# Kernel tuning notes

Hardware: AMD Instinct MI355X
Metric: run time of the kernel (lower is better)

Reference implementation:

```python
import jax, jax.numpy as jnp
import numpy as np

N_NODES = 100000
N_EDGES = 3200000
IN_CH = 128
HID = 16


def setup_inputs() -> dict:
    key = jax.random.key(0)
    ks = jax.random.split(key, 6)
    x = jax.random.normal(ks[0], (N_NODES, IN_CH), dtype=jnp.float32)
    edge_index = jax.random.randint(ks[1], (2, N_EDGES), 0, N_NODES, dtype=jnp.int32)
    W1 = jax.random.normal(ks[2], (IN_CH, HID), dtype=jnp.float32) / np.sqrt(IN_CH)
    b1 = jnp.zeros((HID,), jnp.float32)
    W2 = jax.random.normal(ks[3], (HID, HID), dtype=jnp.float32) / np.sqrt(HID)
    b2 = jnp.zeros((HID,), jnp.float32)
    Wl = jax.random.normal(ks[4], (HID, 1), dtype=jnp.float32) / np.sqrt(HID)
    bl = jnp.zeros((1,), jnp.float32)
    return {"x": x, "edge_index": edge_index, "W1": W1, "b1": b1,
            "W2": W2, "b2": b2, "Wl": Wl, "bl": bl}


def _gcn_conv(x, row, col, dinv, W, b, n_nodes):
    # PyG GCNConv: out[col] += d^{-1/2}[row] * d^{-1/2}[col] * (x @ W)[row]; + bias
    h = x @ W                                   # [N, C_out] small matmul
    norm = dinv[row] * dinv[col]                # [E+N] edge weights (with self-loops)
    msg = h[row] * norm[:, None]                # gather + scale
    out = jax.ops.segment_sum(msg, col, num_segments=n_nodes)  # scatter-add
    return out + b


def reference(x, edge_index, W1, b1, W2, b2, Wl, bl):
    n = x.shape[0]
    loops = jnp.arange(n, dtype=edge_index.dtype)
    row = jnp.concatenate([edge_index[0], loops])  # sources (with self-loops)
    col = jnp.concatenate([edge_index[1], loops])  # targets
    # symmetric normalization degrees computed on A + I at target index
    deg = jax.ops.segment_sum(jnp.ones(col.shape[0], x.dtype), col, num_segments=n)
    dinv = jnp.where(deg > 0, jax.lax.rsqrt(deg), 0.0)
    h = jax.nn.relu(_gcn_conv(x, row, col, dinv, W1, b1, n))
    h = jax.nn.relu(_gcn_conv(h, row, col, dinv, W2, b2, n))
    return h @ Wl + bl
```

## Files before the change

### kernel.cpp

```cpp
#include <hip/hip_runtime.h>

#define IN_CH 128
#define HID 16
#define SHIFT 8
#define CA 16384
#define SCAN_B 512
#define MAXNB 512

typedef int vint4 __attribute__((ext_vector_type(4)));


__global__ __launch_bounds__(256) void histA_kernel(
    const int* __restrict__ col, int* __restrict__ histT, int e, int NB, int nba) {
    __shared__ int hist[MAXNB];
    int j = blockIdx.x, t = threadIdx.x;
    for (int b = t; b < NB; b += 256) hist[b] = 0;
    __syncthreads();
    int e4 = e >> 2;
    const int4* c4p = (const int4*)col;
#pragma unroll
    for (int k = 0; k < CA / 1024; ++k) {
        int i4 = j * (CA / 4) + k * 256 + t;
        if (i4 < e4) {
            int4 c = c4p[i4];
            atomicAdd(&hist[c.x >> SHIFT], 1);
            atomicAdd(&hist[c.y >> SHIFT], 1);
            atomicAdd(&hist[c.z >> SHIFT], 1);
            atomicAdd(&hist[c.w >> SHIFT], 1);
        }
    }
    if (j == gridDim.x - 1) {
        for (int i = (e & ~3) + t; i < e; i += 256) atomicAdd(&hist[col[i] >> SHIFT], 1);
    }
    __syncthreads();
    for (int b = t; b < NB; b += 256) histT[b * nba + j] = hist[b];
}


__global__ __launch_bounds__(SCAN_B) void scan1_kernel(
    const int* __restrict__ in, int* __restrict__ out, int* __restrict__ bsum, int m) {
    __shared__ int s[SCAN_B];
    int t = threadIdx.x;
    int i = blockIdx.x * SCAN_B + t;
    int v = (i < m) ? in[i] : 0;
    s[t] = v;
    __syncthreads();
    for (int off = 1; off < SCAN_B; off <<= 1) {
        int a = (t >= off) ? s[t - off] : 0;
        __syncthreads();
        s[t] += a;
        __syncthreads();
    }
    if (i < m) out[i] = s[t] - v;
    if (t == SCAN_B - 1) bsum[blockIdx.x] = s[t];
}

__global__ __launch_bounds__(SCAN_B) void scan2_kernel(int* __restrict__ bsum, int nb) {
    __shared__ int s[SCAN_B];
    int t = threadIdx.x;
    int v = (t < nb) ? bsum[t] : 0;
    s[t] = v;
    __syncthreads();
    for (int off = 1; off < SCAN_B; off <<= 1) {
        int a = (t >= off) ? s[t - off] : 0;
        __syncthreads();
        s[t] += a;
        __syncthreads();
    }
    if (t < nb) bsum[t] = s[t] - v;
}


__global__ __launch_bounds__(256) void scatterA_kernel(
    const int* __restrict__ row, const int* __restrict__ col,
    const int* __restrict__ histTs, const int* __restrict__ bsum2,
    int* __restrict__ tmp, int e, int NB, int nba) {
    __shared__ int cur[MAXNB];
    int j = blockIdx.x, t = threadIdx.x;
    for (int b = t; b < NB; b += 256) {
        int idx = b * nba + j;
        cur[b] = histTs[idx] + bsum2[idx >> 9];
    }
    __syncthreads();
    int e4 = e >> 2;
    const int4* c4p = (const int4*)col;
    const int4* r4p = (const int4*)row;
#pragma unroll
    for (int k = 0; k < CA / 1024; ++k) {
        int i4 = j * (CA / 4) + k * 256 + t;
        if (i4 < e4) {
            int4 c = c4p[i4];
            int4 r = r4p[i4];
            int pos;
            pos = atomicAdd(&cur[c.x >> SHIFT], 1); tmp[pos] = (r.x << 8) | (c.x & 255);
            pos = atomicAdd(&cur[c.y >> SHIFT], 1); tmp[pos] = (r.y << 8) | (c.y & 255);
            pos = atomicAdd(&cur[c.z >> SHIFT], 1); tmp[pos] = (r.z << 8) | (c.z & 255);
            pos = atomicAdd(&cur[c.w >> SHIFT], 1); tmp[pos] = (r.w << 8) | (c.w & 255);
        }
    }
    if (j == gridDim.x - 1) {
        for (int i = (e & ~3) + t; i < e; i += 256) {
            int c = col[i], r = row[i];
            int pos = atomicAdd(&cur[c >> SHIFT], 1);
            tmp[pos] = (r << 8) | (c & 255);
        }
    }
}


__global__ __launch_bounds__(256) void bucketC_kernel(
    const int* __restrict__ tmp, const int* __restrict__ histTs, const int* __restrict__ bsum2,
    int* __restrict__ row_ptr, int* __restrict__ pcnt, int* __restrict__ bktTot,
    float* __restrict__ dinv, int n, int e, int NB, int nba) {
    __shared__ int hcnt[256];
    __shared__ int scn[256];
    int b = blockIdx.x, t = threadIdx.x;
    int i0 = b * nba, i1 = (b + 1) * nba;
    int bs = histTs[i0] + bsum2[i0 >> 9];
    int be = (b + 1 < NB) ? (histTs[i1] + bsum2[i1 >> 9]) : e;
    hcnt[t] = 0;
    __syncthreads();
    for (int i = bs + t; i < be; i += 256) atomicAdd(&hcnt[tmp[i] & 255], 1);
    __syncthreads();
    int cnt = hcnt[t];
    int pc = (cnt + 7) & ~7;
    scn[t] = pc;
    __syncthreads();
    for (int off = 1; off < 256; off <<= 1) {
        int a = (t >= off) ? scn[t - off] : 0;
        __syncthreads();
        scn[t] += a;
        __syncthreads();
    }
    int excl = scn[t] - pc;
    int node = (b << SHIFT) + t;
    if (node < n) {
        row_ptr[node] = excl;
        pcnt[node] = pc;
        dinv[node] = rsqrtf((float)(cnt + 1));
    }
    if (t == 255) bktTot[b] = scn[255];
    if (b == 0 && t == 0) dinv[n] = 0.0f;
}

__global__ __launch_bounds__(SCAN_B) void scanB_kernel(
    int* __restrict__ bktTot, int* __restrict__ row_ptr, int NB, int n) {
    __shared__ int s[SCAN_B];
    int t = threadIdx.x;
    int v = (t < NB) ? bktTot[t] : 0;
    s[t] = v;
    __syncthreads();
    for (int off = 1; off < SCAN_B; off <<= 1) {
        int a = (t >= off) ? s[t - off] : 0;
        __syncthreads();
        s[t] += a;
        __syncthreads();
    }
    if (t < NB) bktTot[t] = s[t] - v;
    if (t == SCAN_B - 1) row_ptr[n] = s[t];
}


__global__ __launch_bounds__(256) void bucketD_kernel(
    const int* __restrict__ tmp, const int* __restrict__ histTs, const int* __restrict__ bsum2,
    const int* __restrict__ bktTot, const int* __restrict__ pcnt,
    int* __restrict__ row_ptr, int* __restrict__ pk,
    int n, int e, int NB, int nba) {
    __shared__ int cur[256];
    int b = blockIdx.x, t = threadIdx.x;
    int i0 = b * nba, i1 = (b + 1) * nba;
    int bs = histTs[i0] + bsum2[i0 >> 9];
    int be = (b + 1 < NB) ? (histTs[i1] + bsum2[i1 >> 9]) : e;
    int node = (b << SHIFT) + t;
    int rp = 0, pc = 0;
    if (node < n) {
        rp = bktTot[b] + row_ptr[node];
        pc = pcnt[node];
        row_ptr[node] = rp;
    }
    cur[t] = rp;
    __syncthreads();
    for (int i = bs + t; i < be; i += 256) {
        int u = tmp[i];
        int pos = atomicAdd(&cur[u & 255], 1);
        pk[pos] = u >> 8;
    }
    __syncthreads();
    int pe = rp + pc;
    for (int p = cur[t]; p < pe; ++p) pk[p] = n;
}


__global__ __launch_bounds__(256) void gemm1_kernel(
    const float* __restrict__ x, const float* __restrict__ W1,
    const float* __restrict__ dinv, float* __restrict__ hs, int n) {
    __shared__ float4 swl[512];
    int t = threadIdx.x;
#pragma unroll
    for (int i = t; i < 512; i += 256) {
        float4 v = ((const float4*)W1)[i];
        int k = i >> 2, q = i & 3;
        int kp = ((k & 31) << 2) | (k >> 5);
        swl[kp * 4 + q] = v;
    }
    __syncthreads();
    int gid = blockIdx.x * 256 + t;
    int r = gid >> 2;
    int sub = gid & 3;
    if (r > n) return;
    float4 xv[8];
    if (r < n) {
        const float4* xp = (const float4*)(x + (size_t)r * IN_CH + sub * 32);
#pragma unroll
        for (int j = 0; j < 8; ++j) xv[j] = xp[j];
    } else {
#pragma unroll
        for (int j = 0; j < 8; ++j) xv[j] = make_float4(0.f, 0.f, 0.f, 0.f);
    }
    float acc[16];
#pragma unroll
    for (int c = 0; c < 16; ++c) acc[c] = 0.f;
#pragma unroll
    for (int j = 0; j < 8; ++j) {
#pragma unroll
        for (int q = 0; q < 4; ++q) {
            int jq = j * 4 + q;
            float xs = (q == 0) ? xv[j].x : (q == 1) ? xv[j].y : (q == 2) ? xv[j].z : xv[j].w;
            const float4* wp = &swl[(jq * 4 + sub) * 4];
            float4 w0 = wp[0], w1 = wp[1], w2 = wp[2], w3 = wp[3];
            acc[0]  = fmaf(xs, w0.x, acc[0]);
            acc[1]  = fmaf(xs, w0.y, acc[1]);
            acc[2]  = fmaf(xs, w0.z, acc[2]);
            acc[3]  = fmaf(xs, w0.w, acc[3]);
            acc[4]  = fmaf(xs, w1.x, acc[4]);
            acc[5]  = fmaf(xs, w1.y, acc[5]);
            acc[6]  = fmaf(xs, w1.z, acc[6]);
            acc[7]  = fmaf(xs, w1.w, acc[7]);
            acc[8]  = fmaf(xs, w2.x, acc[8]);
            acc[9]  = fmaf(xs, w2.y, acc[9]);
            acc[10] = fmaf(xs, w2.z, acc[10]);
            acc[11] = fmaf(xs, w2.w, acc[11]);
            acc[12] = fmaf(xs, w3.x, acc[12]);
            acc[13] = fmaf(xs, w3.y, acc[13]);
            acc[14] = fmaf(xs, w3.z, acc[14]);
            acc[15] = fmaf(xs, w3.w, acc[15]);
        }
    }
#pragma unroll
    for (int c = 0; c < 16; ++c) {
        acc[c] += __shfl_xor(acc[c], 1);
        acc[c] += __shfl_xor(acc[c], 2);
    }
    float dg = dinv[r];
    float4 o;
    o.x = dg * acc[sub * 4 + 0];
    o.y = dg * acc[sub * 4 + 1];
    o.z = dg * acc[sub * 4 + 2];
    o.w = dg * acc[sub * 4 + 3];
    ((float4*)hs)[(size_t)r * 4 + sub] = o;
}


__global__ __launch_bounds__(256) void agg1_kernel(
    const float* __restrict__ hs, const int* __restrict__ row_ptr,
    const int* __restrict__ pk, const float* __restrict__ dinv,
    const float* __restrict__ b1, const float* __restrict__ W2,
    float* __restrict__ hs2, int n) {
    int t = threadIdx.x;
    int node = blockIdx.x * 64 + (t >> 2);
    int sub = t & 3;
    if (node >= n) return;
    const float4* h4 = (const float4*)hs;
    float4 self = h4[(size_t)node * 4 + sub];
    float cx = self.x, cy = self.y, cz = self.z, cw = self.w;
    int beg = __builtin_nontemporal_load(row_ptr + node);
    int end = __builtin_nontemporal_load(row_ptr + node + 1);
    for (int j = beg; j < end; j += 8) {
        vint4 p0 = __builtin_nontemporal_load((const vint4*)(pk + j));
        vint4 p1 = __builtin_nontemporal_load((const vint4*)(pk + j + 4));
        float4 v0 = h4[(size_t)p0.x * 4 + sub];
        float4 v1 = h4[(size_t)p0.y * 4 + sub];
        float4 v2 = h4[(size_t)p0.z * 4 + sub];
        float4 v3 = h4[(size_t)p0.w * 4 + sub];
        float4 v4 = h4[(size_t)p1.x * 4 + sub];
        float4 v5 = h4[(size_t)p1.y * 4 + sub];
        float4 v6 = h4[(size_t)p1.z * 4 + sub];
        float4 v7 = h4[(size_t)p1.w * 4 + sub];
        cx += ((v0.x + v1.x) + (v2.x + v3.x)) + ((v4.x + v5.x) + (v6.x + v7.x));
        cy += ((v0.y + v1.y) + (v2.y + v3.y)) + ((v4.y + v5.y) + (v6.y + v7.y));
        cz += ((v0.z + v1.z) + (v2.z + v3.z)) + ((v4.z + v5.z) + (v6.z + v7.z));
        cw += ((v0.w + v1.w) + (v2.w + v3.w)) + ((v4.w + v5.w) + (v6.w + v7.w));
    }
    float dg = dinv[node];
    float4 b1v = *(const float4*)(b1 + (sub << 2));
    float ax = fmaxf(fmaf(dg, cx, b1v.x), 0.f);
    float ay = fmaxf(fmaf(dg, cy, b1v.y), 0.f);
    float az = fmaxf(fmaf(dg, cz, b1v.z), 0.f);
    float aw = fmaxf(fmaf(dg, cw, b1v.w), 0.f);
    float ox = 0.f, oy = 0.f, oz = 0.f, ow = 0.f;
#pragma unroll
    for (int r = 0; r < 4; ++r) {
        float fx = __shfl_xor(ax, r);
        float fy = __shfl_xor(ay, r);
        float fz = __shfl_xor(az, r);
        float fw = __shfl_xor(aw, r);
        int kb = (sub ^ r) << 2;
        const float* wp = W2 + kb * HID + (sub << 2);
        float4 w0 = *(const float4*)(wp);
        float4 w1 = *(const float4*)(wp + HID);
        float4 w2 = *(const float4*)(wp + 2 * HID);
        float4 w3 = *(const float4*)(wp + 3 * HID);
        ox += fx * w0.x + fy * w1.x + fz * w2.x + fw * w3.x;
        oy += fx * w0.y + fy * w1.y + fz * w2.y + fw * w3.y;
        oz += fx * w0.z + fy * w1.z + fz * w2.z + fw * w3.z;
        ow += fx * w0.w + fy * w1.w + fz * w2.w + fw * w3.w;
    }
    float4 o; o.x = dg * ox; o.y = dg * oy; o.z = dg * oz; o.w = dg * ow;
    ((float4*)hs2)[(size_t)node * 4 + sub] = o;
}

__global__ __launch_bounds__(256) void agg2_kernel(
    const float* __restrict__ hs2, const int* __restrict__ row_ptr,
    const int* __restrict__ pk, const float* __restrict__ dinv,
    const float* __restrict__ b2, const float* __restrict__ Wl,
    const float* __restrict__ bl, float* __restrict__ out, int n) {
    int t = threadIdx.x;
    int node = blockIdx.x * 64 + (t >> 2);
    int sub = t & 3;
    if (node >= n) return;
    const float4* h4 = (const float4*)hs2;
    float4 self = h4[(size_t)node * 4 + sub];
    float cx = self.x, cy = self.y, cz = self.z, cw = self.w;
    int beg = __builtin_nontemporal_load(row_ptr + node);
    int end = __builtin_nontemporal_load(row_ptr + node + 1);
    for (int j = beg; j < end; j += 8) {
        vint4 p0 = __builtin_nontemporal_load((const vint4*)(pk + j));
        vint4 p1 = __builtin_nontemporal_load((const vint4*)(pk + j + 4));
        float4 v0 = h4[(size_t)p0.x * 4 + sub];
        float4 v1 = h4[(size_t)p0.y * 4 + sub];
        float4 v2 = h4[(size_t)p0.z * 4 + sub];
        float4 v3 = h4[(size_t)p0.w * 4 + sub];
        float4 v4 = h4[(size_t)p1.x * 4 + sub];
        float4 v5 = h4[(size_t)p1.y * 4 + sub];
        float4 v6 = h4[(size_t)p1.z * 4 + sub];
        float4 v7 = h4[(size_t)p1.w * 4 + sub];
        cx += ((v0.x + v1.x) + (v2.x + v3.x)) + ((v4.x + v5.x) + (v6.x + v7.x));
        cy += ((v0.y + v1.y) + (v2.y + v3.y)) + ((v4.y + v5.y) + (v6.y + v7.y));
        cz += ((v0.z + v1.z) + (v2.z + v3.z)) + ((v4.z + v5.z) + (v6.z + v7.z));
        cw += ((v0.w + v1.w) + (v2.w + v3.w)) + ((v4.w + v5.w) + (v6.w + v7.w));
    }
    float dg = dinv[node];
    float4 b2v = *(const float4*)(b2 + (sub << 2));
    float4 wlv = *(const float4*)(Wl + (sub << 2));
    float p = fmaxf(fmaf(dg, cx, b2v.x), 0.f) * wlv.x
            + fmaxf(fmaf(dg, cy, b2v.y), 0.f) * wlv.y
            + fmaxf(fmaf(dg, cz, b2v.z), 0.f) * wlv.z
            + fmaxf(fmaf(dg, cw, b2v.w), 0.f) * wlv.w;
    p += __shfl_xor(p, 1);
    p += __shfl_xor(p, 2);
    if (sub == 0) out[node] = p + bl[0];
}

extern "C" void kernel_launch(void* const* d_in, const int* in_sizes, int n_in,
                              void* d_out, int out_size, void* d_ws, size_t ws_size,
                              hipStream_t stream) {
    const float* x  = (const float*)d_in[0];
    const int*   ei = (const int*)d_in[1];
    const float* W1 = (const float*)d_in[2];
    const float* b1 = (const float*)d_in[3];
    const float* W2 = (const float*)d_in[4];
    const float* b2 = (const float*)d_in[5];
    const float* Wl = (const float*)d_in[6];
    const float* bl = (const float*)d_in[7];

    int n = in_sizes[0] / IN_CH;
    int e = in_sizes[1] / 2;
    const int* row = ei;
    const int* col = ei + e;

    int NB  = (n + 255) >> SHIFT;
    int nba = (e + CA - 1) / CA;
    int m   = NB * nba;
    int nsb = (m + SCAN_B - 1) / SCAN_B;

    char* ws = (char*)d_ws;
    size_t off = 0;
    auto alloc = [&](size_t bytes) -> void* {
        void* p = ws + off;
        off = (off + bytes + 255) & ~(size_t)255;
        return p;
    };

    size_t tabf = (size_t)(n + 1) * HID;

    int*   histT   = (int*)alloc((size_t)m * 4);
    int*   histTs  = (int*)alloc((size_t)m * 4);
    int*   bsum2   = (int*)alloc((size_t)nsb * 4);
    int*   row_ptr = (int*)alloc(((size_t)n + 1) * 4);
    int*   pcnt    = (int*)alloc((size_t)n * 4);
    int*   bktTot  = (int*)alloc((size_t)NB * 4);
    float* dinv    = (float*)alloc(((size_t)n + 1) * 4);
    int*   pk      = (int*)alloc(((size_t)e + 8 * (size_t)n + 64) * 4);
    size_t region = (size_t)e * 4;
    size_t tables = 2 * tabf * 4;
    char*  R      = (char*)alloc(region > tables ? region : tables);
    int*   tmp    = (int*)R;
    float* hs     = (float*)R;
    float* hs2    = hs + tabf;

    dim3 blk(256);
    dim3 gG((4 * (n + 1) + 255) / 256);
    dim3 gA((n + 63) / 64);

    hipLaunchKernelGGL(histA_kernel,    dim3(nba), blk, 0, stream, col, histT, e, NB, nba);
    hipLaunchKernelGGL(scan1_kernel,    dim3(nsb), dim3(SCAN_B), 0, stream, histT, histTs, bsum2, m);
    hipLaunchKernelGGL(scan2_kernel,    dim3(1),   dim3(SCAN_B), 0, stream, bsum2, nsb);
    hipLaunchKernelGGL(scatterA_kernel, dim3(nba), blk, 0, stream, row, col, histTs, bsum2, tmp, e, NB, nba);
    hipLaunchKernelGGL(bucketC_kernel,  dim3(NB),  blk, 0, stream, tmp, histTs, bsum2, row_ptr, pcnt, bktTot, dinv, n, e, NB, nba);
    hipLaunchKernelGGL(scanB_kernel,    dim3(1),   dim3(SCAN_B), 0, stream, bktTot, row_ptr, NB, n);
    hipLaunchKernelGGL(bucketD_kernel,  dim3(NB),  blk, 0, stream, tmp, histTs, bsum2, bktTot, pcnt, row_ptr, pk, n, e, NB, nba);

    hipLaunchKernelGGL(gemm1_kernel, gG, blk, 0, stream, x, W1, dinv, hs, n);
    hipLaunchKernelGGL(agg1_kernel,  gA, blk, 0, stream, hs, row_ptr, pk, dinv, b1, W2, hs2, n);
    hipLaunchKernelGGL(agg2_kernel,  gA, blk, 0, stream, hs2, row_ptr, pk, dinv, b2, Wl, bl, (float*)d_out, n);
}
```

Baseline: 168.9 us.

## Split aggregation neighbor lists across two thread quads with prefetched indices

Both aggregation kernels now give each node 8 threads instead of 4. The two quads take alternating 8-edge chunks and combine their partial sums with a cross-lane shuffle. The next chunk's packed indices are also prefetched before the current chunk's gathers are issued, so more gathers are in flight per node. This doubles thread count and adds shuffle overhead, and a quad whose first chunk is already past the row end does no useful work.

```diff
diff --git a/kernel.cpp b/kernel.cpp
--- a/kernel.cpp
+++ b/kernel.cpp
@@ -261,36 +261,56 @@
 }
 
 
+#define AGG_GATHER_LOOP                                                          \
+    int beg = __builtin_nontemporal_load(row_ptr + node);                        \
+    int end = __builtin_nontemporal_load(row_ptr + node + 1);                    \
+    int j = beg + (qd << 3);                                                     \
+    vint4 p0, p1;                                                                \
+    if (j < end) {                                                               \
+        p0 = __builtin_nontemporal_load((const vint4*)(pk + j));                 \
+        p1 = __builtin_nontemporal_load((const vint4*)(pk + j + 4));             \
+    }                                                                            \
+    while (j < end) {                                                            \
+        int jn = j + 16;                                                         \
+        vint4 q0, q1;                                                            \
+        if (jn < end) {                                                          \
+            q0 = __builtin_nontemporal_load((const vint4*)(pk + jn));            \
+            q1 = __builtin_nontemporal_load((const vint4*)(pk + jn + 4));        \
+        }                                                                        \
+        float4 v0 = h4[(size_t)p0.x * 4 + sub];                                  \
+        float4 v1 = h4[(size_t)p0.y * 4 + sub];                                  \
+        float4 v2 = h4[(size_t)p0.z * 4 + sub];                                  \
+        float4 v3 = h4[(size_t)p0.w * 4 + sub];                                  \
+        float4 v4 = h4[(size_t)p1.x * 4 + sub];                                  \
+        float4 v5 = h4[(size_t)p1.y * 4 + sub];                                  \
+        float4 v6 = h4[(size_t)p1.z * 4 + sub];                                  \
+        float4 v7 = h4[(size_t)p1.w * 4 + sub];                                  \
+        cx += ((v0.x + v1.x) + (v2.x + v3.x)) + ((v4.x + v5.x) + (v6.x + v7.x)); \
+        cy += ((v0.y + v1.y) + (v2.y + v3.y)) + ((v4.y + v5.y) + (v6.y + v7.y)); \
+        cz += ((v0.z + v1.z) + (v2.z + v3.z)) + ((v4.z + v5.z) + (v6.z + v7.z)); \
+        cw += ((v0.w + v1.w) + (v2.w + v3.w)) + ((v4.w + v5.w) + (v6.w + v7.w)); \
+        p0 = q0; p1 = q1; j = jn;                                                \
+    }                                                                            \
+    cx += __shfl_xor(cx, 4);                                                     \
+    cy += __shfl_xor(cy, 4);                                                     \
+    cz += __shfl_xor(cz, 4);                                                     \
+    cw += __shfl_xor(cw, 4);
+
 __global__ __launch_bounds__(256) void agg1_kernel(
     const float* __restrict__ hs, const int* __restrict__ row_ptr,
     const int* __restrict__ pk, const float* __restrict__ dinv,
     const float* __restrict__ b1, const float* __restrict__ W2,
     float* __restrict__ hs2, int n) {
     int t = threadIdx.x;
-    int node = blockIdx.x * 64 + (t >> 2);
+    int node = blockIdx.x * 32 + (t >> 3);
     int sub = t & 3;
+    int qd  = (t >> 2) & 1;
     if (node >= n) return;
     const float4* h4 = (const float4*)hs;
     float4 self = h4[(size_t)node * 4 + sub];
-    float cx = self.x, cy = self.y, cz = self.z, cw = self.w;
-    int beg = __builtin_nontemporal_load(row_ptr + node);
-    int end = __builtin_nontemporal_load(row_ptr + node + 1);
-    for (int j = beg; j < end; j += 8) {
-        vint4 p0 = __builtin_nontemporal_load((const vint4*)(pk + j));
-        vint4 p1 = __builtin_nontemporal_load((const vint4*)(pk + j + 4));
-        float4 v0 = h4[(size_t)p0.x * 4 + sub];
-        float4 v1 = h4[(size_t)p0.y * 4 + sub];
-        float4 v2 = h4[(size_t)p0.z * 4 + sub];
-        float4 v3 = h4[(size_t)p0.w * 4 + sub];
-        float4 v4 = h4[(size_t)p1.x * 4 + sub];
-        float4 v5 = h4[(size_t)p1.y * 4 + sub];
-        float4 v6 = h4[(size_t)p1.z * 4 + sub];
-        float4 v7 = h4[(size_t)p1.w * 4 + sub];
-        cx += ((v0.x + v1.x) + (v2.x + v3.x)) + ((v4.x + v5.x) + (v6.x + v7.x));
-        cy += ((v0.y + v1.y) + (v2.y + v3.y)) + ((v4.y + v5.y) + (v6.y + v7.y));
-        cz += ((v0.z + v1.z) + (v2.z + v3.z)) + ((v4.z + v5.z) + (v6.z + v7.z));
-        cw += ((v0.w + v1.w) + (v2.w + v3.w)) + ((v4.w + v5.w) + (v6.w + v7.w));
-    }
+    float cx = qd ? 0.f : self.x, cy = qd ? 0.f : self.y;
+    float cz = qd ? 0.f : self.z, cw = qd ? 0.f : self.w;
+    AGG_GATHER_LOOP
     float dg = dinv[node];
     float4 b1v = *(const float4*)(b1 + (sub << 2));
     float ax = fmaxf(fmaf(dg, cx, b1v.x), 0.f);
@@ -315,8 +335,10 @@
         oz += fx * w0.z + fy * w1.z + fz * w2.z + fw * w3.z;
         ow += fx * w0.w + fy * w1.w + fz * w2.w + fw * w3.w;
     }
-    float4 o; o.x = dg * ox; o.y = dg * oy; o.z = dg * oz; o.w = dg * ow;
-    ((float4*)hs2)[(size_t)node * 4 + sub] = o;
+    if (qd == 0) {
+        float4 o; o.x = dg * ox; o.y = dg * oy; o.z = dg * oz; o.w = dg * ow;
+        ((float4*)hs2)[(size_t)node * 4 + sub] = o;
+    }
 }
 
 __global__ __launch_bounds__(256) void agg2_kernel(
@@ -325,30 +347,15 @@
     const float* __restrict__ b2, const float* __restrict__ Wl,
     const float* __restrict__ bl, float* __restrict__ out, int n) {
     int t = threadIdx.x;
-    int node = blockIdx.x * 64 + (t >> 2);
+    int node = blockIdx.x * 32 + (t >> 3);
     int sub = t & 3;
+    int qd  = (t >> 2) & 1;
     if (node >= n) return;
     const float4* h4 = (const float4*)hs2;
     float4 self = h4[(size_t)node * 4 + sub];
-    float cx = self.x, cy = self.y, cz = self.z, cw = self.w;
-    int beg = __builtin_nontemporal_load(row_ptr + node);
-    int end = __builtin_nontemporal_load(row_ptr + node + 1);
-    for (int j = beg; j < end; j += 8) {
-        vint4 p0 = __builtin_nontemporal_load((const vint4*)(pk + j));
-        vint4 p1 = __builtin_nontemporal_load((const vint4*)(pk + j + 4));
-        float4 v0 = h4[(size_t)p0.x * 4 + sub];
-        float4 v1 = h4[(size_t)p0.y * 4 + sub];
-        float4 v2 = h4[(size_t)p0.z * 4 + sub];
-        float4 v3 = h4[(size_t)p0.w * 4 + sub];
-        float4 v4 = h4[(size_t)p1.x * 4 + sub];
-        float4 v5 = h4[(size_t)p1.y * 4 + sub];
-        float4 v6 = h4[(size_t)p1.z * 4 + sub];
-        float4 v7 = h4[(size_t)p1.w * 4 + sub];
-        cx += ((v0.x + v1.x) + (v2.x + v3.x)) + ((v4.x + v5.x) + (v6.x + v7.x));
-        cy += ((v0.y + v1.y) + (v2.y + v3.y)) + ((v4.y + v5.y) + (v6.y + v7.y));
-        cz += ((v0.z + v1.z) + (v2.z + v3.z)) + ((v4.z + v5.z) + (v6.z + v7.z));
-        cw += ((v0.w + v1.w) + (v2.w + v3.w)) + ((v4.w + v5.w) + (v6.w + v7.w));
-    }
+    float cx = qd ? 0.f : self.x, cy = qd ? 0.f : self.y;
+    float cz = qd ? 0.f : self.z, cw = qd ? 0.f : self.w;
+    AGG_GATHER_LOOP
     float dg = dinv[node];
     float4 b2v = *(const float4*)(b2 + (sub << 2));
     float4 wlv = *(const float4*)(Wl + (sub << 2));
@@ -358,7 +365,7 @@
             + fmaxf(fmaf(dg, cw, b2v.w), 0.f) * wlv.w;
     p += __shfl_xor(p, 1);
     p += __shfl_xor(p, 2);
-    if (sub == 0) out[node] = p + bl[0];
+    if ((t & 7) == 0) out[node] = p + bl[0];
 }
 
 extern "C" void kernel_launch(void* const* d_in, const int* in_sizes, int n_in,
@@ -410,7 +417,7 @@
 
     dim3 blk(256);
     dim3 gG((4 * (n + 1) + 255) / 256);
-    dim3 gA((n + 63) / 64);
+    dim3 gA((8 * n + 255) / 256);
 
     hipLaunchKernelGGL(histA_kernel,    dim3(nba), blk, 0, stream, col, histT, e, NB, nba);
     hipLaunchKernelGGL(scan1_kernel,    dim3(nsb), dim3(SCAN_B), 0, stream, histT, histTs, bsum2, m);
```

Measured after the change: 154.7 us. 8.4% less time.
